# Kernel tuning notes

Measured on AMD Instinct MI355X. Metric: run time of the kernel, lower is better.

Reference implementation:

```python
import jax, jax.numpy as jnp
import numpy as np

B, N, E_PER = 2048, 64, 512            # graphs, nodes/graph, edges/graph
D_NODE, D_EMB = 16, 64                 # env.node_state_dim, node_embedding_size
D_USER, D_UEMB = 32, 64                # env.user_state_dim, user_embedding_size
HID = 512
TOTAL_N, TOTAL_E = B * N, B * E_PER


def setup_inputs() -> dict:
    key = jax.random.key(0)
    ks = jax.random.split(key, 16)
    off = (jnp.arange(B, dtype=jnp.int32) * N)[:, None]
    src = jax.random.randint(ks[0], (B, E_PER), 0, N, dtype=jnp.int32) + off
    dst = jax.random.randint(ks[1], (B, E_PER), 0, N, dtype=jnp.int32) + off
    edge_index = jnp.stack([src.reshape(-1), dst.reshape(-1)])  # [2, TOTAL_E]
    s = lambda k, shape, sc=0.05: jax.random.normal(k, shape, jnp.float32) * sc
    return {
        "x": jax.random.normal(ks[2], (TOTAL_N, D_NODE), jnp.float32),
        "edge_attr": jax.random.normal(ks[3], (TOTAL_E, 2), jnp.float32),
        "user_s": jax.random.normal(ks[4], (B, D_USER), jnp.float32),
        "W_msg": s(ks[5], (D_NODE, D_EMB)), "b_msg": jnp.zeros((D_EMB,), jnp.float32),
        "W_edge": s(ks[6], (2, D_EMB)),     "b_edge": jnp.zeros((D_EMB,), jnp.float32),
        "W_self": s(ks[7], (D_NODE, D_EMB)),"b_self": jnp.zeros((D_EMB,), jnp.float32),
        "W1": s(ks[8], (D_USER, D_UEMB)),   "b1": jnp.zeros((D_UEMB,), jnp.float32),
        "W2": s(ks[9], (N * D_EMB + D_UEMB, HID)), "b2": jnp.zeros((HID,), jnp.float32),
        "W3": s(ks[10], (HID, HID // 2)),   "b3": jnp.zeros((HID // 2,), jnp.float32),
        "W4": s(ks[11], (HID // 2, N), 0.01), "b4": jnp.zeros((N,), jnp.float32),
        "edge_index": edge_index,
    }


def reference(x, edge_attr, user_s, W_msg, b_msg, W_edge, b_edge, W_self, b_self,
              W1, b1, W2, b2, W3, b3, W4, b4, edge_index):
    src, dst = edge_index[0], edge_index[1]
    # GeneralConv (PyG): msg = lin_msg(x_j) + lin_edge(e); sum-aggregate at dst; + lin_self(x_i)
    msg = x[src] @ W_msg + b_msg + edge_attr @ W_edge + b_edge          # [TOTAL_E, D_EMB]
    agg = jax.ops.segment_sum(msg, dst, num_segments=TOTAL_N)          # [TOTAL_N, D_EMB]
    node = jax.nn.relu(agg + x @ W_self + b_self)
    # F.dropout(p=0.5, training=True) -- deterministic mask for the reference
    keep = jax.random.bernoulli(jax.random.key(42), 0.5, node.shape)
    node = jnp.where(keep, node * 2.0, 0.0)
    user = jax.nn.relu(user_s @ W1 + b1)                               # [B, D_UEMB]
    states = jnp.concatenate([node.reshape(B, N * D_EMB), user], axis=1)
    h = jax.nn.relu(states @ W2 + b2)
    h = jax.nn.relu(h @ W3 + b3)
    logits = h @ W4 + b4                                               # [B, N]
    # torch: unsqueeze(dim=0) then softmax(dim=1) => softmax across the BATCH axis
    return jax.nn.softmax(logits, axis=0)[None]                        # [1, B, N]
```

## Files before the change

### kernel.cpp

```cpp
#include <hip/hip_runtime.h>
#include <stdint.h>

#define B_GRAPHS 2048
#define CHUNK 256
#define E_PER 512
#define D_USER 32
#define HID 512
#define GK 4160
#define STATES_DIM 4160
#define WS_FALLBACK 6356992
#define WS_FAST 32051200

typedef unsigned short u16;
typedef unsigned int u32;
typedef __attribute__((ext_vector_type(8))) short short8;
typedef __attribute__((ext_vector_type(4))) float f32x4;

__device__ __forceinline__ float bf2f(u16 b) {
    union { uint32_t u; float f; } c; c.u = ((uint32_t)b) << 16; return c.f;
}
__device__ __forceinline__ u16 f2bf(float f) {
    union { float f; uint32_t u; } c; c.f = f;
    uint32_t u = c.u;
    return (u16)((u + 0x7FFFu + ((u >> 16) & 1u)) >> 16);
}
__device__ __forceinline__ void unpack2(uint32_t w, float& lo, float& hi) {
    union { uint32_t u; float f; } a, b;
    a.u = w << 16; b.u = w & 0xFFFF0000u;
    lo = a.f; hi = b.f;
}

__device__ __forceinline__ uint32_t rotl32(uint32_t v, int r) {
    return (v << r) | (v >> (32 - r));
}
__device__ __forceinline__ void threefry_0_42(uint32_t x0, uint32_t x1,
                                              uint32_t& o0, uint32_t& o1) {
    const uint32_t ks0 = 0u, ks1 = 42u, ks2 = 0x1BD11BDAu ^ 42u;
    x0 += ks0; x1 += ks1;
#define TFR(r) { x0 += x1; x1 = rotl32(x1, (r)); x1 ^= x0; }
    TFR(13) TFR(15) TFR(26) TFR(6)
    x0 += ks1; x1 += ks2 + 1u;
    TFR(17) TFR(29) TFR(16) TFR(24)
    x0 += ks2; x1 += ks0 + 2u;
    TFR(13) TFR(15) TFR(26) TFR(6)
    x0 += ks0; x1 += ks1 + 3u;
    TFR(17) TFR(29) TFR(16) TFR(24)
    x0 += ks1; x1 += ks2 + 4u;
    TFR(13) TFR(15) TFR(26) TFR(6)
    x0 += ks2; x1 += ks0 + 5u;
#undef TFR
    o0 = x0; o1 = x1;
}
__device__ __forceinline__ bool keep_bit(uint32_t j) {
    uint32_t o0, o1;
    threefry_0_42(0u, j, o0, o1);
    return (((o0 ^ o1) >> 31) == 0u);
}

__global__ __launch_bounds__(256) void mask_kernel(unsigned long long* __restrict__ mask) {
    uint32_t j = blockIdx.x * 256u + threadIdx.x;
    uint32_t o0, o1;
    threefry_0_42(0u, j, o0, o1);
    unsigned long long b = __ballot(((o0 ^ o1) >> 31) == 0u);
    if ((threadIdx.x & 63u) == 0u) mask[j >> 6] = b;
}

__global__ __launch_bounds__(256) void fill_kernel(float* __restrict__ out, float v, int n) {
    int i = blockIdx.x * 256 + threadIdx.x;
    if (i < n) out[i] = v;
}

__global__ __launch_bounds__(256) void prep_wcat(
    const float* __restrict__ W_msg, const float* __restrict__ W_self,
    u16* __restrict__ WcatT)
{
    int t = threadIdx.x;
    #pragma unroll
    for (int i = 0; i < 8; ++i) {
        int idx = t + 256 * i;
        int e = idx >> 5, k = idx & 31;
        float v = (k < 16) ? W_msg[k * 64 + e] : W_self[(k - 16) * 64 + e];
        WcatT[idx] = f2bf(v);
    }
}

__global__ __launch_bounds__(256) void node_fast(
    const float* __restrict__ x, const float* __restrict__ edge_attr,
    const float* __restrict__ user_s,
    const float* __restrict__ W_msg, const float* __restrict__ b_msg,
    const float* __restrict__ W_edge, const float* __restrict__ b_edge,
    const float* __restrict__ W_self, const float* __restrict__ b_self,
    const float* __restrict__ W1, const float* __restrict__ b1,
    const int* __restrict__ src, const int* __restrict__ dst,
    const unsigned long long* __restrict__ mask,
    const u16* __restrict__ WcatT,
    u16* __restrict__ states)
{
    const int g = blockIdx.x;
    const int tid = threadIdx.x;
    const int w = tid >> 6, lane = tid & 63;
    const int lm = lane & 15, q = lane >> 4;

    __shared__ u32 scntp[64][32];
    __shared__ u16 cntbf[64][72];
    __shared__ u16 sxT[16][72];
    __shared__ u16 sA2[64][40];
    __shared__ float sesum[2][64];
    __shared__ float sdeg[64];
    __shared__ unsigned long long smask[64];

    const float* xg = x + (size_t)g * 1024;
    float xv[4];
    #pragma unroll
    for (int i = 0; i < 4; ++i) xv[i] = xg[tid + 256 * i];
    const int ge0 = g * E_PER + tid, ge1 = ge0 + 256;
    const int s0 = src[ge0] - g * 64, d0 = dst[ge0] - g * 64;
    const int s1 = src[ge1] - g * 64, d1 = dst[ge1] - g * 64;
    const float2* ea2 = (const float2*)edge_attr;
    const float2 a0 = ea2[ge0], a1 = ea2[ge1];
    float bs[4], bm[4], we0[4], we1[4];
    #pragma unroll
    for (int nt = 0; nt < 4; ++nt) {
        int e = nt * 16 + lm;
        bs[nt]  = b_self[e];
        bm[nt]  = b_msg[e] + b_edge[e];
        we0[nt] = W_edge[e];
        we1[nt] = W_edge[64 + e];
    }
    {
        uint4 z = make_uint4(0, 0, 0, 0);
        u32* c0 = &scntp[0][0] + tid * 8;
        *(uint4*)(c0) = z; *(uint4*)(c0 + 4) = z;
    }
    if (tid < 128) ((float*)sesum)[tid] = 0.f;
    if (tid < 64) smask[tid] = mask[g * 64 + tid];
    #pragma unroll
    for (int i = 0; i < 4; ++i) {
        int idx = tid + 256 * i;
        int n = idx >> 4, k = idx & 15;
        u16 bv = f2bf(xv[i]);
        sxT[k][n] = bv;
        sA2[n][16 + k] = bv;
    }
    __syncthreads();

    atomicAdd(&scntp[d0][s0 >> 1], 1u << ((s0 & 1) * 16));
    atomicAdd(&scntp[d1][s1 >> 1], 1u << ((s1 & 1) * 16));
    atomicAdd(&sesum[0][d0], a0.x);
    atomicAdd(&sesum[1][d0], a0.y);
    atomicAdd(&sesum[0][d1], a1.x);
    atomicAdd(&sesum[1][d1], a1.y);
    __syncthreads();

    {
        const int d = tid >> 2, sq = tid & 3;
        uint4 c0 = *(const uint4*)&scntp[d][sq * 8];
        uint4 c1 = *(const uint4*)&scntp[d][sq * 8 + 4];
        u32 cw[8] = {c0.x, c0.y, c0.z, c0.w, c1.x, c1.y, c1.z, c1.w};
        u32 pk[8];
        float degp = 0.f;
        #pragma unroll
        for (int j = 0; j < 8; ++j) {
            u32 lo = cw[j] & 0xFFFFu, hi = cw[j] >> 16;
            degp += (float)(lo + hi);
            pk[j] = (u32)f2bf((float)lo) | ((u32)f2bf((float)hi) << 16);
        }
        uint4 o0 = make_uint4(pk[0], pk[1], pk[2], pk[3]);
        uint4 o1 = make_uint4(pk[4], pk[5], pk[6], pk[7]);
        *(uint4*)&cntbf[d][sq * 16]     = o0;
        *(uint4*)&cntbf[d][sq * 16 + 8] = o1;
        degp += __shfl_xor(degp, 1, 64);
        degp += __shfl_xor(degp, 2, 64);
        if (sq == 0) sdeg[d] = degp;
    }
    __syncthreads();

    f32x4 accS;
    #pragma unroll
    for (int r = 0; r < 4; ++r) accS[r] = 0.f;
    #pragma unroll
    for (int kh = 0; kh < 2; ++kh) {
        short8 a = *(const short8*)&cntbf[16 * w + lm][kh * 32 + q * 8];
        short8 b = *(const short8*)&sxT[lm][kh * 32 + q * 8];
        accS = __builtin_amdgcn_mfma_f32_16x16x32_bf16(a, b, accS, 0, 0, 0);
    }
    #pragma unroll
    for (int r = 0; r < 4; ++r)
        sA2[16 * w + q * 4 + r][lm] = f2bf(accS[r]);

    f32x4 acc2[4];
    #pragma unroll
    for (int nt = 0; nt < 4; ++nt)
        #pragma unroll
        for (int r = 0; r < 4; ++r) acc2[nt][r] = 0.f;
    short8 a2 = *(const short8*)&sA2[16 * w + lm][q * 8];
    #pragma unroll
    for (int nt = 0; nt < 4; ++nt) {
        short8 b2 = *(const short8*)&WcatT[(nt * 16 + lm) * 32 + q * 8];
        acc2[nt] = __builtin_amdgcn_mfma_f32_16x16x32_bf16(a2, b2, acc2[nt], 0, 0, 0);
    }

    u16* out = states + (size_t)g * STATES_DIM;
    #pragma unroll
    for (int r = 0; r < 4; ++r) {
        int n = 16 * w + q * 4 + r;
        float dg = sdeg[n], e0 = sesum[0][n], e1 = sesum[1][n];
        unsigned long long m = smask[n];
        #pragma unroll
        for (int nt = 0; nt < 4; ++nt) {
            float v = acc2[nt][r] + bs[nt] + dg * bm[nt]
                    + e0 * we0[nt] + e1 * we1[nt];
            v = v > 0.f ? v : 0.f;
            int e = nt * 16 + lm;
            v = ((m >> e) & 1ull) ? v * 2.0f : 0.0f;
            out[n * 64 + e] = f2bf(v);
        }
    }
    if (tid < 64) {
        float v = b1[tid];
        const float* us = user_s + (size_t)g * D_USER;
        #pragma unroll
        for (int k = 0; k < D_USER; ++k) v += us[k] * W1[k * 64 + tid];
        out[4096 + tid] = f2bf(v > 0.f ? v : 0.f);
    }
}

__global__ __launch_bounds__(256) void node_fb(
    int g0,
    const float* __restrict__ x, const float* __restrict__ edge_attr,
    const float* __restrict__ user_s,
    const float* __restrict__ W_msg, const float* __restrict__ b_msg,
    const float* __restrict__ W_edge, const float* __restrict__ b_edge,
    const float* __restrict__ W_self, const float* __restrict__ b_self,
    const float* __restrict__ W1, const float* __restrict__ b1,
    const int* __restrict__ src, const int* __restrict__ dst,
    float* __restrict__ states)
{
    const int g = g0 + blockIdx.x;
    const int tid = threadIdx.x;

    __shared__ float sx[64][16];
    __shared__ float sxsum[64][16];
    __shared__ float sesum[64][2];
    __shared__ float sdeg[64];
    __shared__ float sWmsg[16][64];
    __shared__ float sWself[16][64];
    __shared__ float sWedge[2][64];
    __shared__ float sbias[64];
    __shared__ float sbself[64];

    const float* xg = x + (size_t)g * 1024;
    for (int i = tid; i < 1024; i += 256) {
        sx[i >> 4][i & 15] = xg[i];
        ((float*)sxsum)[i] = 0.f;
        ((float*)sWmsg)[i] = W_msg[i];
        ((float*)sWself)[i] = W_self[i];
    }
    if (tid < 128) ((float*)sWedge)[tid] = W_edge[tid];
    if (tid < 64) {
        sbias[tid] = b_msg[tid] + b_edge[tid];
        sbself[tid] = b_self[tid];
        sdeg[tid] = 0.f;
        sesum[tid][0] = 0.f; sesum[tid][1] = 0.f;
    }
    __syncthreads();

    const float2* ea2 = (const float2*)edge_attr;
    for (int e = tid; e < E_PER; e += 256) {
        int ge = g * E_PER + e;
        int s = src[ge] - g * 64;
        int d = dst[ge] - g * 64;
        float2 a = ea2[ge];
        atomicAdd(&sdeg[d], 1.0f);
        atomicAdd(&sesum[d][0], a.x);
        atomicAdd(&sesum[d][1], a.y);
        #pragma unroll
        for (int k = 0; k < 16; ++k) atomicAdd(&sxsum[d][k], sx[s][k]);
    }
    __syncthreads();

    float* out = states + (size_t)blockIdx.x * STATES_DIM;
    #pragma unroll
    for (int i = 0; i < 16; ++i) {
        int idx = tid + 256 * i;
        int n = idx >> 6, e = idx & 63;
        float v = sbself[e] + sdeg[n] * sbias[e]
                + sesum[n][0] * sWedge[0][e] + sesum[n][1] * sWedge[1][e];
        #pragma unroll
        for (int k = 0; k < 16; ++k)
            v += sxsum[n][k] * sWmsg[k][e] + sx[n][k] * sWself[k][e];
        v = v > 0.f ? v : 0.f;
        v = keep_bit((uint32_t)g * 4096u + (uint32_t)idx) ? v * 2.0f : 0.0f;
        out[idx] = v;
    }
    if (tid < 64) {
        float v = b1[tid];
        const float* us = user_s + (size_t)g * D_USER;
        #pragma unroll
        for (int k = 0; k < D_USER; ++k) v += us[k] * W1[k * 64 + tid];
        out[4096 + tid] = v > 0.f ? v : 0.f;
    }
}

__global__ __launch_bounds__(256) void transpose_w(const float* __restrict__ W,
                                                   u16* __restrict__ WT,
                                                   int K, int N) {
    __shared__ float sT[32][33];
    const int k0 = blockIdx.x * 32, n0 = blockIdx.y * 32;
    const int tr = threadIdx.x >> 5, tc = threadIdx.x & 31;
    #pragma unroll
    for (int i = 0; i < 32; i += 8)
        sT[tr + i][tc] = W[(size_t)(k0 + tr + i) * N + n0 + tc];
    __syncthreads();
    #pragma unroll
    for (int i = 0; i < 32; i += 8)
        WT[(size_t)(n0 + tr + i) * K + k0 + tc] = f2bf(sT[tc][tr + i]);
}

__global__ __launch_bounds__(256) void gemm_splitk(
    const u16* __restrict__ A, const u16* __restrict__ BT,
    float* __restrict__ Cacc, int K, int Ksplit, int N)
{
    const int bid = blockIdx.x;
    const int j = bid >> 3;
    const int mt = (bid & 7) * 8 + (j & 7);
    const int nt = j >> 3;
    const int m0 = mt * 32, n0 = nt * 64;
    const int kb = blockIdx.y * Ksplit;

    __shared__ u16 sA[32][72];
    __shared__ u16 sB[64][72];

    const int tid = threadIdx.x;
    const int wave = tid >> 6, lane = tid & 63;
    const int wm = (wave & 1) * 16, wn = (wave >> 1) * 32;
    const int lm = lane & 15, q = lane >> 4;

    f32x4 acc0, acc1;
    #pragma unroll
    for (int r = 0; r < 4; ++r) { acc0[r] = 0.f; acc1[r] = 0.f; }

    const int arow = tid >> 3, aseg = (tid & 7) * 8;
    const int brow = tid >> 2, bseg = (tid & 3) * 16;

    const u16* pa = &A [(size_t)(m0 + arow) * K + kb + aseg];
    const u16* pb = &BT[(size_t)(n0 + brow) * K + kb + bseg];
    uint4 ra  = *(const uint4*)pa;
    uint4 rb0 = *(const uint4*)pb, rb1 = *(const uint4*)(pb + 8);

    for (int k0 = 0; k0 < Ksplit; k0 += 64) {
        __syncthreads();
        *(uint4*)&sA[arow][aseg]     = ra;
        *(uint4*)&sB[brow][bseg]     = rb0;
        *(uint4*)&sB[brow][bseg + 8] = rb1;
        __syncthreads();
        if (k0 + 64 < Ksplit) {
            pa += 64; pb += 64;
            ra  = *(const uint4*)pa;
            rb0 = *(const uint4*)pb; rb1 = *(const uint4*)(pb + 8);
        }
        #pragma unroll
        for (int kh = 0; kh < 2; ++kh) {
            short8 a  = *(const short8*)&sA[wm + lm][kh * 32 + q * 8];
            short8 b0 = *(const short8*)&sB[wn + lm][kh * 32 + q * 8];
            short8 b1 = *(const short8*)&sB[wn + 16 + lm][kh * 32 + q * 8];
            acc0 = __builtin_amdgcn_mfma_f32_16x16x32_bf16(a, b0, acc0, 0, 0, 0);
            acc1 = __builtin_amdgcn_mfma_f32_16x16x32_bf16(a, b1, acc1, 0, 0, 0);
        }
    }

    #pragma unroll
    for (int r = 0; r < 4; ++r) {
        int m = m0 + wm + q * 4 + r;
        atomicAdd(&Cacc[(size_t)m * N + n0 + wn + lm],      acc0[r]);
        atomicAdd(&Cacc[(size_t)m * N + n0 + wn + 16 + lm], acc1[r]);
    }
}

__global__ __launch_bounds__(256) void bias_relu_cast(
    const float* __restrict__ acc, const float* __restrict__ bias,
    u16* __restrict__ out, int Nmask, int total)
{
    int i = blockIdx.x * 256 + threadIdx.x;
    if (i < total) {
        float v = acc[i] + bias[i & Nmask];
        out[i] = f2bf(v > 0.f ? v : 0.f);
    }
}

template<typename AT, typename CT, bool RELU>
__global__ __launch_bounds__(256) void gemm_any(
    const AT* __restrict__ A, const float* __restrict__ B,
    const float* __restrict__ bias, CT* __restrict__ C,
    int M, int N, int K)
{
    __shared__ float sA[32][72];
    __shared__ float sB[32][64];

    const int tid = threadIdx.x;
    const int tx = tid & 15;
    const int ty = tid >> 4;
    const int m0 = blockIdx.x * 64, n0 = blockIdx.y * 64;

    float acc[4][4] = {};

    for (int k0 = 0; k0 < K; k0 += 32) {
        if constexpr (sizeof(AT) == 4) {
            int r = tid >> 3;
            int c = (tid & 7) * 4;
            #pragma unroll
            for (int rr = 0; rr < 64; rr += 32) {
                float4 v = *(const float4*)&((const float*)A)[(size_t)(m0 + r + rr) * K + k0 + c];
                sA[c + 0][r + rr] = v.x; sA[c + 1][r + rr] = v.y;
                sA[c + 2][r + rr] = v.z; sA[c + 3][r + rr] = v.w;
            }
        } else {
            int m = tid >> 2;
            int c = (tid & 3) * 8;
            uint4 v = *(const uint4*)&((const u16*)A)[(size_t)(m0 + m) * K + k0 + c];
            unpack2(v.x, sA[c + 0][m], sA[c + 1][m]);
            unpack2(v.y, sA[c + 2][m], sA[c + 3][m]);
            unpack2(v.z, sA[c + 4][m], sA[c + 5][m]);
            unpack2(v.w, sA[c + 6][m], sA[c + 7][m]);
        }
        {
            int r = tid >> 3;
            int nc = (tid & 7) * 8;
            float4 v0 = *(const float4*)&B[(size_t)(k0 + r) * N + n0 + nc];
            float4 v1 = *(const float4*)&B[(size_t)(k0 + r) * N + n0 + nc + 4];
            sB[r][nc + 0] = v0.x; sB[r][nc + 1] = v0.y;
            sB[r][nc + 2] = v0.z; sB[r][nc + 3] = v0.w;
            sB[r][nc + 4] = v1.x; sB[r][nc + 5] = v1.y;
            sB[r][nc + 6] = v1.z; sB[r][nc + 7] = v1.w;
        }
        __syncthreads();
        #pragma unroll
        for (int kk = 0; kk < 32; ++kk) {
            float4 av = *(const float4*)&sA[kk][ty * 4];
            float4 bv = *(const float4*)&sB[kk][tx * 4];
            float a_[4] = {av.x, av.y, av.z, av.w};
            float b_[4] = {bv.x, bv.y, bv.z, bv.w};
            #pragma unroll
            for (int i = 0; i < 4; ++i)
                #pragma unroll
                for (int j = 0; j < 4; ++j)
                    acc[i][j] += a_[i] * b_[j];
        }
        __syncthreads();
    }

    #pragma unroll
    for (int i = 0; i < 4; ++i) {
        int m = m0 + ty * 4 + i;
        #pragma unroll
        for (int j = 0; j < 4; ++j) {
            int n = n0 + tx * 4 + j;
            float v = acc[i][j] + bias[n];
            if (RELU) v = v > 0.f ? v : 0.f;
            if constexpr (sizeof(CT) == 2) C[(size_t)m * N + n] = (CT)f2bf(v);
            else                           C[(size_t)m * N + n] = (CT)v;
        }
    }
}

__global__ __launch_bounds__(256) void softmax_kernel(
    const float* __restrict__ logits, float* __restrict__ out)
{
    const int n = blockIdx.x;
    const int tid = threadIdx.x;
    __shared__ float sred[4];
    const int wid = tid >> 6, lane = tid & 63;

    float v[8];
    #pragma unroll
    for (int i = 0; i < 8; ++i) {
        float t = logits[(tid + 256 * i) * 64 + n];
        v[i] = (t > -1e30f && t < 1e30f) ? t : 0.0f;
    }

    float mx = -3.4e38f;
    #pragma unroll
    for (int i = 0; i < 8; ++i) mx = fmaxf(mx, v[i]);
    #pragma unroll
    for (int off = 32; off > 0; off >>= 1) mx = fmaxf(mx, __shfl_down(mx, off, 64));
    if (lane == 0) sred[wid] = mx;
    __syncthreads();
    if (tid == 0) sred[0] = fmaxf(fmaxf(sred[0], sred[1]), fmaxf(sred[2], sred[3]));
    __syncthreads();
    mx = sred[0];
    __syncthreads();

    float sum = 0.f;
    #pragma unroll
    for (int i = 0; i < 8; ++i) { v[i] = expf(v[i] - mx); sum += v[i]; }
    #pragma unroll
    for (int off = 32; off > 0; off >>= 1) sum += __shfl_down(sum, off, 64);
    if (lane == 0) sred[wid] = sum;
    __syncthreads();
    if (tid == 0) sred[0] = sred[0] + sred[1] + sred[2] + sred[3];
    __syncthreads();
    float inv = 1.0f / sred[0];
    #pragma unroll
    for (int i = 0; i < 8; ++i) out[(tid + 256 * i) * 64 + n] = v[i] * inv;
}

extern "C" void kernel_launch(void* const* d_in, const int* in_sizes, int n_in,
                              void* d_out, int out_size, void* d_ws, size_t ws_size,
                              hipStream_t stream) {
    if (ws_size < (size_t)WS_FALLBACK || n_in < 18) {
        fill_kernel<<<(out_size + 255) / 256, 256, 0, stream>>>((float*)d_out, 0.25f, out_size);
        return;
    }
    {
        const int expect[18] = {2097152, 2097152, 65536, 1024, 64, 128, 64,
                                1024, 64, 2048, 64, 2129920, 512, 131072, 256,
                                16384, 64, 2097152};
        bool ok = true;
        for (int i = 0; i < 18; ++i) ok = ok && (in_sizes[i] == expect[i]);
        if (!ok || out_size != 131072) {
            fill_kernel<<<(out_size + 255) / 256, 256, 0, stream>>>((float*)d_out, 0.125f, out_size);
            return;
        }
    }

    const float* x         = (const float*)d_in[0];
    const float* edge_attr = (const float*)d_in[1];
    const float* user_s    = (const float*)d_in[2];
    const float* W_msg     = (const float*)d_in[3];
    const float* b_msg     = (const float*)d_in[4];
    const float* W_edge    = (const float*)d_in[5];
    const float* b_edge    = (const float*)d_in[6];
    const float* W_self    = (const float*)d_in[7];
    const float* b_self    = (const float*)d_in[8];
    const float* W1        = (const float*)d_in[9];
    const float* b1        = (const float*)d_in[10];
    const float* W2        = (const float*)d_in[11];
    const float* b2        = (const float*)d_in[12];
    const float* W3        = (const float*)d_in[13];
    const float* b3        = (const float*)d_in[14];
    const float* W4        = (const float*)d_in[15];
    const float* b4        = (const float*)d_in[16];
    const int* edge_index  = (const int*)d_in[17];
    const int* src = edge_index;
    const int* dst = edge_index + B_GRAPHS * E_PER;

    float* logits = (float*)d_out;
    char* ws = (char*)d_ws;

    if (ws_size >= (size_t)WS_FAST) {
        u16*   states = (u16*)ws;
        u16*   W2T    = (u16*)(ws + 17039360);
        unsigned long long* mask = (unsigned long long*)(ws + 21299200);
        float* h2acc  = (float*)(ws + 22347776);
        u16*   h2     = (u16*)(ws + 26542080);
        u16*   W3T    = (u16*)(ws + 28639232);
        float* h3acc  = (float*)(ws + 28901376);
        u16*   h3     = (u16*)(ws + 30998528);
        u16*   WcatT  = (u16*)(ws + 32047104);

        mask_kernel<<<32768, 256, 0, stream>>>(mask);
        prep_wcat<<<1, 256, 0, stream>>>(W_msg, W_self, WcatT);
        node_fast<<<B_GRAPHS, 256, 0, stream>>>(
            x, edge_attr, user_s, W_msg, b_msg, W_edge, b_edge,
            W_self, b_self, W1, b1, src, dst, mask, WcatT, states);
        transpose_w<<<dim3(130, 16), 256, 0, stream>>>(W2, W2T, GK, 512);
        fill_kernel<<<4096, 256, 0, stream>>>(h2acc, 0.f, B_GRAPHS * HID);
        gemm_splitk<<<dim3(512, 5), 256, 0, stream>>>(states, W2T, h2acc,
                                                      GK, 832, 512);
        bias_relu_cast<<<4096, 256, 0, stream>>>(h2acc, b2, h2, 511,
                                                 B_GRAPHS * HID);
        transpose_w<<<dim3(16, 8), 256, 0, stream>>>(W3, W3T, 512, 256);
        fill_kernel<<<2048, 256, 0, stream>>>(h3acc, 0.f, B_GRAPHS * 256);
        gemm_splitk<<<dim3(256, 2), 256, 0, stream>>>(h2, W3T, h3acc,
                                                      512, 256, 256);
        bias_relu_cast<<<2048, 256, 0, stream>>>(h3acc, b3, h3, 255,
                                                 B_GRAPHS * 256);
        gemm_any<u16, float, false><<<dim3(32, 1), 256, 0, stream>>>(
            h3, W4, b4, logits, B_GRAPHS, 64, 256);
        softmax_kernel<<<64, 256, 0, stream>>>(logits, logits);
    } else {
        float* states = (float*)ws;
        float* h3     = (float*)ws;
        u16*   h2     = (u16*)(ws + 4259840);

        for (int c = 0; c < B_GRAPHS / CHUNK; ++c) {
            node_fb<<<CHUNK, 256, 0, stream>>>(
                c * CHUNK, x, edge_attr, user_s, W_msg, b_msg, W_edge, b_edge,
                W_self, b_self, W1, b1, src, dst, states);
            gemm_any<float, u16, true><<<dim3(CHUNK / 64, HID / 64), 256, 0, stream>>>(
                states, W2, b2, h2 + (size_t)c * CHUNK * HID, CHUNK, HID, STATES_DIM);
        }
        gemm_any<u16,   float, true ><<<dim3(32, 4), 256, 0, stream>>>(
            h2, W3, b3, h3, B_GRAPHS, HID / 2, HID);
        gemm_any<float, float, false><<<dim3(32, 1), 256, 0, stream>>>(
            h3, W4, b4, logits, B_GRAPHS, 64, HID / 2);
        softmax_kernel<<<64, 256, 0, stream>>>(logits, logits);
    }
}
```

Before: 207.9 us.

## Use 64x64 split-K GEMM tiles with partial buffers, fuse small prep kernels

The split-K GEMMs move from 32x64 tiles with atomic float accumulation to 64x64 tiles. Each split writes its own partial buffer, and a vectorized bias+ReLU+sum kernel then reduces the partials. This drops the zero-fill kernels and atomic traffic but enlarges the workspace and adds partial-buffer reads. The Wcat prep is folded into the mask kernel as an extra block to save a launch. Inside node_fast, the count matrix is converted to bf16 in place with an XOR swizzle, which removes a shared buffer and a barrier, and x is loaded as float4.

```diff
diff --git a/kernel.cpp b/kernel.cpp
--- a/kernel.cpp
+++ b/kernel.cpp
@@ -9,7 +9,7 @@
 #define GK 4160
 #define STATES_DIM 4160
 #define WS_FALLBACK 6356992
-#define WS_FAST 32051200
+#define WS_FAST 50925568
 
 typedef unsigned short u16;
 typedef unsigned int u32;
@@ -57,7 +57,22 @@
     return (((o0 ^ o1) >> 31) == 0u);
 }
 
-__global__ __launch_bounds__(256) void mask_kernel(unsigned long long* __restrict__ mask) {
+__global__ __launch_bounds__(256) void mask_wcat_kernel(
+    unsigned long long* __restrict__ mask,
+    const float* __restrict__ W_msg, const float* __restrict__ W_self,
+    u16* __restrict__ WcatT)
+{
+    if (blockIdx.x == 32768) {
+        int t = threadIdx.x;
+        #pragma unroll
+        for (int i = 0; i < 8; ++i) {
+            int idx = t + 256 * i;
+            int e = idx >> 5, k = idx & 31;
+            float v = (k < 16) ? W_msg[k * 64 + e] : W_self[(k - 16) * 64 + e];
+            WcatT[idx] = f2bf(v);
+        }
+        return;
+    }
     uint32_t j = blockIdx.x * 256u + threadIdx.x;
     uint32_t o0, o1;
     threefry_0_42(0u, j, o0, o1);
@@ -70,26 +85,11 @@
     if (i < n) out[i] = v;
 }
 
-__global__ __launch_bounds__(256) void prep_wcat(
-    const float* __restrict__ W_msg, const float* __restrict__ W_self,
-    u16* __restrict__ WcatT)
-{
-    int t = threadIdx.x;
-    #pragma unroll
-    for (int i = 0; i < 8; ++i) {
-        int idx = t + 256 * i;
-        int e = idx >> 5, k = idx & 31;
-        float v = (k < 16) ? W_msg[k * 64 + e] : W_self[(k - 16) * 64 + e];
-        WcatT[idx] = f2bf(v);
-    }
-}
-
 __global__ __launch_bounds__(256) void node_fast(
     const float* __restrict__ x, const float* __restrict__ edge_attr,
     const float* __restrict__ user_s,
-    const float* __restrict__ W_msg, const float* __restrict__ b_msg,
-    const float* __restrict__ W_edge, const float* __restrict__ b_edge,
-    const float* __restrict__ W_self, const float* __restrict__ b_self,
+    const float* __restrict__ b_msg, const float* __restrict__ W_edge,
+    const float* __restrict__ b_edge, const float* __restrict__ b_self,
     const float* __restrict__ W1, const float* __restrict__ b1,
     const int* __restrict__ src, const int* __restrict__ dst,
     const unsigned long long* __restrict__ mask,
@@ -101,8 +101,7 @@
     const int w = tid >> 6, lane = tid & 63;
     const int lm = lane & 15, q = lane >> 4;
 
-    __shared__ u32 scntp[64][32];
-    __shared__ u16 cntbf[64][72];
+    __shared__ u32 scnt[64][32];
     __shared__ u16 sxT[16][72];
     __shared__ u16 sA2[64][40];
     __shared__ float sesum[2][64];
@@ -110,9 +109,7 @@
     __shared__ unsigned long long smask[64];
 
     const float* xg = x + (size_t)g * 1024;
-    float xv[4];
-    #pragma unroll
-    for (int i = 0; i < 4; ++i) xv[i] = xg[tid + 256 * i];
+    const float4 xv = *(const float4*)&xg[tid * 4];
     const int ge0 = g * E_PER + tid, ge1 = ge0 + 256;
     const int s0 = src[ge0] - g * 64, d0 = dst[ge0] - g * 64;
     const int s1 = src[ge1] - g * 64, d1 = dst[ge1] - g * 64;
@@ -129,23 +126,22 @@
     }
     {
         uint4 z = make_uint4(0, 0, 0, 0);
-        u32* c0 = &scntp[0][0] + tid * 8;
+        u32* c0 = &scnt[0][0] + tid * 8;
         *(uint4*)(c0) = z; *(uint4*)(c0 + 4) = z;
     }
     if (tid < 128) ((float*)sesum)[tid] = 0.f;
     if (tid < 64) smask[tid] = mask[g * 64 + tid];
-    #pragma unroll
-    for (int i = 0; i < 4; ++i) {
-        int idx = tid + 256 * i;
-        int n = idx >> 4, k = idx & 15;
-        u16 bv = f2bf(xv[i]);
-        sxT[k][n] = bv;
-        sA2[n][16 + k] = bv;
-    }
-    __syncthreads();
-
-    atomicAdd(&scntp[d0][s0 >> 1], 1u << ((s0 & 1) * 16));
-    atomicAdd(&scntp[d1][s1 >> 1], 1u << ((s1 & 1) * 16));
+    {
+        const int n = tid >> 2, kb = (tid & 3) * 4;
+        u16 x0 = f2bf(xv.x), x1 = f2bf(xv.y), x2 = f2bf(xv.z), x3 = f2bf(xv.w);
+        sxT[kb + 0][n] = x0; sxT[kb + 1][n] = x1;
+        sxT[kb + 2][n] = x2; sxT[kb + 3][n] = x3;
+        *(ushort4*)&sA2[n][16 + kb] = make_ushort4(x0, x1, x2, x3);
+    }
+    __syncthreads();
+
+    atomicAdd(&scnt[d0][(s0 >> 1) ^ ((d0 & 7) << 2)], 1u << ((s0 & 1) * 16));
+    atomicAdd(&scnt[d1][(s1 >> 1) ^ ((d1 & 7) << 2)], 1u << ((s1 & 1) * 16));
     atomicAdd(&sesum[0][d0], a0.x);
     atomicAdd(&sesum[1][d0], a0.y);
     atomicAdd(&sesum[0][d1], a1.x);
@@ -154,8 +150,8 @@
 
     {
         const int d = tid >> 2, sq = tid & 3;
-        uint4 c0 = *(const uint4*)&scntp[d][sq * 8];
-        uint4 c1 = *(const uint4*)&scntp[d][sq * 8 + 4];
+        uint4 c0 = *(const uint4*)&scnt[d][sq * 8];
+        uint4 c1 = *(const uint4*)&scnt[d][sq * 8 + 4];
         u32 cw[8] = {c0.x, c0.y, c0.z, c0.w, c1.x, c1.y, c1.z, c1.w};
         u32 pk[8];
         float degp = 0.f;
@@ -165,24 +161,25 @@
             degp += (float)(lo + hi);
             pk[j] = (u32)f2bf((float)lo) | ((u32)f2bf((float)hi) << 16);
         }
-        uint4 o0 = make_uint4(pk[0], pk[1], pk[2], pk[3]);
-        uint4 o1 = make_uint4(pk[4], pk[5], pk[6], pk[7]);
-        *(uint4*)&cntbf[d][sq * 16]     = o0;
-        *(uint4*)&cntbf[d][sq * 16 + 8] = o1;
+        *(uint4*)&scnt[d][sq * 8]     = make_uint4(pk[0], pk[1], pk[2], pk[3]);
+        *(uint4*)&scnt[d][sq * 8 + 4] = make_uint4(pk[4], pk[5], pk[6], pk[7]);
         degp += __shfl_xor(degp, 1, 64);
         degp += __shfl_xor(degp, 2, 64);
         if (sq == 0) sdeg[d] = degp;
     }
-    __syncthreads();
 
     f32x4 accS;
     #pragma unroll
     for (int r = 0; r < 4; ++r) accS[r] = 0.f;
-    #pragma unroll
-    for (int kh = 0; kh < 2; ++kh) {
-        short8 a = *(const short8*)&cntbf[16 * w + lm][kh * 32 + q * 8];
-        short8 b = *(const short8*)&sxT[lm][kh * 32 + q * 8];
-        accS = __builtin_amdgcn_mfma_f32_16x16x32_bf16(a, b, accS, 0, 0, 0);
+    {
+        const char* crow = (const char*)&scnt[16 * w + lm][0];
+        const int sw = (lm & 7) << 4;
+        #pragma unroll
+        for (int kh = 0; kh < 2; ++kh) {
+            short8 a = *(const short8*)(crow + (((kh * 64) + q * 16) ^ sw));
+            short8 b = *(const short8*)&sxT[lm][kh * 32 + q * 8];
+            accS = __builtin_amdgcn_mfma_f32_16x16x32_bf16(a, b, accS, 0, 0, 0);
+        }
     }
     #pragma unroll
     for (int r = 0; r < 4; ++r)
@@ -317,75 +314,93 @@
         WT[(size_t)(n0 + tr + i) * K + k0 + tc] = f2bf(sT[tc][tr + i]);
 }
 
-__global__ __launch_bounds__(256) void gemm_splitk(
+__global__ __launch_bounds__(256) void gemm64(
     const u16* __restrict__ A, const u16* __restrict__ BT,
-    float* __restrict__ Cacc, int K, int Ksplit, int N)
+    float* __restrict__ Cpart, int K, int Ksplit, int N, int ntiles,
+    int pstride)
 {
+    const int cpx = gridDim.x >> 3;
     const int bid = blockIdx.x;
-    const int j = bid >> 3;
-    const int mt = (bid & 7) * 8 + (j & 7);
-    const int nt = j >> 3;
-    const int m0 = mt * 32, n0 = nt * 64;
+    const int wg  = (bid & 7) * cpx + (bid >> 3);
+    const int nt  = wg % ntiles, mt = wg / ntiles;
+    const int m0 = mt * 64, n0 = nt * 64;
     const int kb = blockIdx.y * Ksplit;
 
-    __shared__ u16 sA[32][72];
+    __shared__ u16 sA[64][72];
     __shared__ u16 sB[64][72];
 
     const int tid = threadIdx.x;
     const int wave = tid >> 6, lane = tid & 63;
-    const int wm = (wave & 1) * 16, wn = (wave >> 1) * 32;
+    const int wm = (wave & 1) * 32, wn = (wave >> 1) * 32;
     const int lm = lane & 15, q = lane >> 4;
 
-    f32x4 acc0, acc1;
-    #pragma unroll
-    for (int r = 0; r < 4; ++r) { acc0[r] = 0.f; acc1[r] = 0.f; }
-
-    const int arow = tid >> 3, aseg = (tid & 7) * 8;
-    const int brow = tid >> 2, bseg = (tid & 3) * 16;
-
+    f32x4 acc00, acc01, acc10, acc11;
+    #pragma unroll
+    for (int r = 0; r < 4; ++r) {
+        acc00[r] = 0.f; acc01[r] = 0.f; acc10[r] = 0.f; acc11[r] = 0.f;
+    }
+
+    const int arow = tid >> 2, aseg = (tid & 3) * 16;
     const u16* pa = &A [(size_t)(m0 + arow) * K + kb + aseg];
-    const u16* pb = &BT[(size_t)(n0 + brow) * K + kb + bseg];
-    uint4 ra  = *(const uint4*)pa;
+    const u16* pb = &BT[(size_t)(n0 + arow) * K + kb + aseg];
+    uint4 ra0 = *(const uint4*)pa, ra1 = *(const uint4*)(pa + 8);
     uint4 rb0 = *(const uint4*)pb, rb1 = *(const uint4*)(pb + 8);
 
     for (int k0 = 0; k0 < Ksplit; k0 += 64) {
         __syncthreads();
-        *(uint4*)&sA[arow][aseg]     = ra;
-        *(uint4*)&sB[brow][bseg]     = rb0;
-        *(uint4*)&sB[brow][bseg + 8] = rb1;
+        *(uint4*)&sA[arow][aseg]     = ra0;
+        *(uint4*)&sA[arow][aseg + 8] = ra1;
+        *(uint4*)&sB[arow][aseg]     = rb0;
+        *(uint4*)&sB[arow][aseg + 8] = rb1;
         __syncthreads();
         if (k0 + 64 < Ksplit) {
             pa += 64; pb += 64;
-            ra  = *(const uint4*)pa;
+            ra0 = *(const uint4*)pa; ra1 = *(const uint4*)(pa + 8);
             rb0 = *(const uint4*)pb; rb1 = *(const uint4*)(pb + 8);
         }
         #pragma unroll
         for (int kh = 0; kh < 2; ++kh) {
-            short8 a  = *(const short8*)&sA[wm + lm][kh * 32 + q * 8];
-            short8 b0 = *(const short8*)&sB[wn + lm][kh * 32 + q * 8];
+            short8 a0 = *(const short8*)&sA[wm + lm]     [kh * 32 + q * 8];
+            short8 a1 = *(const short8*)&sA[wm + 16 + lm][kh * 32 + q * 8];
+            short8 b0 = *(const short8*)&sB[wn + lm]     [kh * 32 + q * 8];
             short8 b1 = *(const short8*)&sB[wn + 16 + lm][kh * 32 + q * 8];
-            acc0 = __builtin_amdgcn_mfma_f32_16x16x32_bf16(a, b0, acc0, 0, 0, 0);
-            acc1 = __builtin_amdgcn_mfma_f32_16x16x32_bf16(a, b1, acc1, 0, 0, 0);
-        }
-    }
-
+            acc00 = __builtin_amdgcn_mfma_f32_16x16x32_bf16(a0, b0, acc00, 0, 0, 0);
+            acc01 = __builtin_amdgcn_mfma_f32_16x16x32_bf16(a0, b1, acc01, 0, 0, 0);
+            acc10 = __builtin_amdgcn_mfma_f32_16x16x32_bf16(a1, b0, acc10, 0, 0, 0);
+            acc11 = __builtin_amdgcn_mfma_f32_16x16x32_bf16(a1, b1, acc11, 0, 0, 0);
+        }
+    }
+
+    float* Cp = Cpart + (size_t)blockIdx.y * pstride;
     #pragma unroll
     for (int r = 0; r < 4; ++r) {
         int m = m0 + wm + q * 4 + r;
-        atomicAdd(&Cacc[(size_t)m * N + n0 + wn + lm],      acc0[r]);
-        atomicAdd(&Cacc[(size_t)m * N + n0 + wn + 16 + lm], acc1[r]);
-    }
-}
-
-__global__ __launch_bounds__(256) void bias_relu_cast(
-    const float* __restrict__ acc, const float* __restrict__ bias,
-    u16* __restrict__ out, int Nmask, int total)
+        Cp[(size_t)m * N + n0 + wn + lm]              = acc00[r];
+        Cp[(size_t)m * N + n0 + wn + 16 + lm]         = acc01[r];
+        Cp[(size_t)(m + 16) * N + n0 + wn + lm]       = acc10[r];
+        Cp[(size_t)(m + 16) * N + n0 + wn + 16 + lm]  = acc11[r];
+    }
+}
+
+__global__ __launch_bounds__(256) void bias_relu_sum(
+    const float* __restrict__ parts, int pstride, int nsplit,
+    const float* __restrict__ bias, u16* __restrict__ out,
+    int Nmask, int total4)
 {
     int i = blockIdx.x * 256 + threadIdx.x;
-    if (i < total) {
-        float v = acc[i] + bias[i & Nmask];
-        out[i] = f2bf(v > 0.f ? v : 0.f);
-    }
+    if (i >= total4) return;
+    const int base = i * 4;
+    float4 v = *(const float4*)&bias[base & Nmask];
+    for (int s = 0; s < nsplit; ++s) {
+        float4 p = *(const float4*)&parts[(size_t)s * pstride + base];
+        v.x += p.x; v.y += p.y; v.z += p.z; v.w += p.w;
+    }
+    ushort4 o;
+    o.x = f2bf(v.x > 0.f ? v.x : 0.f);
+    o.y = f2bf(v.y > 0.f ? v.y : 0.f);
+    o.z = f2bf(v.z > 0.f ? v.z : 0.f);
+    o.w = f2bf(v.w > 0.f ? v.w : 0.f);
+    *(ushort4*)&out[base] = o;
 }
 
 template<typename AT, typename CT, bool RELU>
@@ -551,30 +566,27 @@
         u16*   states = (u16*)ws;
         u16*   W2T    = (u16*)(ws + 17039360);
         unsigned long long* mask = (unsigned long long*)(ws + 21299200);
-        float* h2acc  = (float*)(ws + 22347776);
-        u16*   h2     = (u16*)(ws + 26542080);
-        u16*   W3T    = (u16*)(ws + 28639232);
-        float* h3acc  = (float*)(ws + 28901376);
-        u16*   h3     = (u16*)(ws + 30998528);
-        u16*   WcatT  = (u16*)(ws + 32047104);
-
-        mask_kernel<<<32768, 256, 0, stream>>>(mask);
-        prep_wcat<<<1, 256, 0, stream>>>(W_msg, W_self, WcatT);
+        float* h2part = (float*)(ws + 22347776);
+        u16*   h2     = (u16*)(ws + 43319296);
+        u16*   W3T    = (u16*)(ws + 45416448);
+        float* h3part = (float*)(ws + 45678592);
+        u16*   h3     = (u16*)(ws + 49872896);
+        u16*   WcatT  = (u16*)(ws + 50921472);
+
+        mask_wcat_kernel<<<32769, 256, 0, stream>>>(mask, W_msg, W_self, WcatT);
         node_fast<<<B_GRAPHS, 256, 0, stream>>>(
-            x, edge_attr, user_s, W_msg, b_msg, W_edge, b_edge,
-            W_self, b_self, W1, b1, src, dst, mask, WcatT, states);
+            x, edge_attr, user_s, b_msg, W_edge, b_edge, b_self, W1, b1,
+            src, dst, mask, WcatT, states);
         transpose_w<<<dim3(130, 16), 256, 0, stream>>>(W2, W2T, GK, 512);
-        fill_kernel<<<4096, 256, 0, stream>>>(h2acc, 0.f, B_GRAPHS * HID);
-        gemm_splitk<<<dim3(512, 5), 256, 0, stream>>>(states, W2T, h2acc,
-                                                      GK, 832, 512);
-        bias_relu_cast<<<4096, 256, 0, stream>>>(h2acc, b2, h2, 511,
-                                                 B_GRAPHS * HID);
+        gemm64<<<dim3(256, 5), 256, 0, stream>>>(states, W2T, h2part,
+                                                 GK, 832, 512, 8, 1048576);
+        bias_relu_sum<<<1024, 256, 0, stream>>>(h2part, 1048576, 5, b2, h2,
+                                                511, 262144);
         transpose_w<<<dim3(16, 8), 256, 0, stream>>>(W3, W3T, 512, 256);
-        fill_kernel<<<2048, 256, 0, stream>>>(h3acc, 0.f, B_GRAPHS * 256);
-        gemm_splitk<<<dim3(256, 2), 256, 0, stream>>>(h2, W3T, h3acc,
-                                                      512, 256, 256);
-        bias_relu_cast<<<2048, 256, 0, stream>>>(h3acc, b3, h3, 255,
-                                                 B_GRAPHS * 256);
+        gemm64<<<dim3(128, 2), 256, 0, stream>>>(h2, W3T, h3part,
+                                                 512, 256, 256, 4, 524288);
+        bias_relu_sum<<<512, 256, 0, stream>>>(h3part, 524288, 2, b3, h3,
+                                               255, 131072);
         gemm_any<u16, float, false><<<dim3(32, 1), 256, 0, stream>>>(
             h3, W4, b4, logits, B_GRAPHS, 64, 256);
         softmax_kernel<<<64, 256, 0, stream>>>(logits, logits);
```

Measured after the change: 192.5 us. 1.08x faster.
